# Optimization experiments

Measured on AMD Instinct MI355X. Metric: run time of the kernel, lower is better.

## Reference

```python
import jax, jax.numpy as jnp
import numpy as np

B, N, E, F, FE = 4, 10000, 160000, 128, 16  # batch, nodes, edges, filters(=node feat dim), edge feat dim
EPS = 1e-3  # keras LayerNormalization default epsilon


def layernorm(x, gamma, beta):
    mu = jnp.mean(x, axis=-1, keepdims=True)
    var = jnp.mean(jnp.square(x - mu), axis=-1, keepdims=True)
    return (x - mu) * jax.lax.rsqrt(var + EPS) * gamma + beta


def setup_inputs() -> dict:
    key = jax.random.key(0)
    ks = jax.random.split(key, 8)
    nodes = jax.random.normal(ks[0], (B, N, F), dtype=jnp.float32)
    edge_features = jax.random.normal(ks[1], (B, E, FE), dtype=jnp.float32)
    edges = jax.random.randint(ks[2], (B, E, 2), 0, N, dtype=jnp.int32)
    edge_weights = jax.random.uniform(ks[3], (B, E, 1), dtype=jnp.float32)
    edge_dropout = jnp.ones((B, E, 2), dtype=jnp.float32)
    W_msg = jax.random.normal(ks[4], (2 * F + FE, F), dtype=jnp.float32) * 0.02
    b_msg = jnp.zeros((F,), jnp.float32)
    g_msg = jnp.ones((F,), jnp.float32)
    beta_msg = jnp.zeros((F,), jnp.float32)
    W_upd = jax.random.normal(ks[5], (2 * F, F), dtype=jnp.float32) * 0.02
    b_upd = jnp.zeros((F,), jnp.float32)
    g_upd = jnp.ones((F,), jnp.float32)
    beta_upd = jnp.zeros((F,), jnp.float32)
    return dict(nodes=nodes, edge_features=edge_features, edges=edges,
                edge_weights=edge_weights, edge_dropout=edge_dropout,
                W_msg=W_msg, b_msg=b_msg, g_msg=g_msg, beta_msg=beta_msg,
                W_upd=W_upd, b_upd=b_upd, g_upd=g_upd, beta_upd=beta_upd)


def reference(nodes, edge_features, edges, edge_weights, edge_dropout,
              W_msg, b_msg, g_msg, beta_msg, W_upd, b_upd, g_upd, beta_upd):
    n = nodes.shape[1]
    # gather both endpoints per edge: [B,E,2,F] -> [B,E,2F]
    gathered = jax.vmap(lambda nd, ed: nd[ed])(nodes, edges)
    msg_in = gathered.reshape(gathered.shape[0], gathered.shape[1], -1)
    msg_in = jnp.concatenate([msg_in, edge_features], axis=-1)
    # message MLP: Dense + GELU + LayerNorm
    h = jnp.einsum('bei,io->beo', msg_in, W_msg) + b_msg
    messages = layernorm(jax.nn.gelu(h, approximate=False), g_msg, beta_msg)
    weighted_messages = messages * edge_weights
    # scatter-sum to destination nodes (edge[:,1]), masked by dropout col 1
    dropped = weighted_messages * edge_dropout[..., 1:2]
    dst = edges[..., 1]
    aggregated = jax.vmap(lambda m, d: jax.ops.segment_sum(m, d, num_segments=n))(dropped, dst)
    # update: concat + Dense + GELU + LayerNorm
    combined = jnp.concatenate([nodes, aggregated], axis=-1)
    u = jnp.einsum('bni,io->bno', combined, W_upd) + b_upd
    updated_nodes = layernorm(jax.nn.gelu(u, approximate=False), g_upd, beta_upd)
    return updated_nodes
```

## Files before the change

kernel.cpp:

```cpp
#include <hip/hip_runtime.h>
#include <hip/hip_bf16.h>
#include <hip/hip_fp16.h>

#define BATCH   4
#define NNODES  10000
#define NEDGES  160000
#define FDIM    128
#define FEDIM   16
#define LNEPS   1e-3f

typedef __attribute__((ext_vector_type(8))) short v8s;
typedef __attribute__((ext_vector_type(4))) float v4f;

#define AGG_BYTES   ((size_t)BATCH * NNODES * FDIM * 2)
#define P_OFF       AGG_BYTES
#define P_BYTES     ((size_t)BATCH * NNODES * 256 * 2)
#define WTCAT_OFF   (P_OFF + P_BYTES)
#define WTUPD_OFF   (WTCAT_OFF + (size_t)256 * 128 * 2)
#define W3T_OFF     (WTUPD_OFF + (size_t)128 * 256 * 2)

static __device__ __forceinline__ unsigned short f2bf(float f) {
    __hip_bfloat16 h = __float2bfloat16(f);
    return *reinterpret_cast<unsigned short*>(&h);
}
static __device__ __forceinline__ float bfbits2f(unsigned bits16) {
    return __uint_as_float(bits16 << 16);
}

static __device__ __forceinline__ float gelu_f(float x) {
    float z = 0.7978845608028654f * (x + 0.044715f * x * x * x);
    float e = __expf(2.0f * z);
    float t = 1.0f - 2.0f / (e + 1.0f);
    return 0.5f * x * (1.0f + t);
}

static __device__ __forceinline__ bool is_bf16_mode(const void* gflag) {
    return ((*reinterpret_cast<const unsigned*>(gflag)) & 0xFFFFu) != 0u;
}
static __device__ __forceinline__ float ld_f(const void* p, long i, bool bf) {
    return bf ? (float)reinterpret_cast<const __hip_bfloat16*>(p)[i]
              : reinterpret_cast<const float*>(p)[i];
}
static __device__ __forceinline__ uint4 pack8(const float* p) {
    float4 f0 = *reinterpret_cast<const float4*>(p);
    float4 f1 = *reinterpret_cast<const float4*>(p + 4);
    uint4 o;
    o.x = f2bf(f0.x) | ((unsigned)f2bf(f0.y) << 16);
    o.y = f2bf(f0.z) | ((unsigned)f2bf(f0.w) << 16);
    o.z = f2bf(f1.x) | ((unsigned)f2bf(f1.y) << 16);
    o.w = f2bf(f1.z) | ((unsigned)f2bf(f1.w) << 16);
    return o;
}
static __device__ __forceinline__ uint4 h8_to_bf8(uint4 u) {
    unsigned w[4] = {u.x, u.y, u.z, u.w};
    uint4 o; unsigned r[4];
    #pragma unroll
    for (int q = 0; q < 4; q++) {
        __half lo = *reinterpret_cast<const __half*>(&w[q]);
        unsigned short hib = (unsigned short)(w[q] >> 16);
        __half hi = *reinterpret_cast<const __half*>(&hib);
        r[q] = f2bf(__half2float(lo)) | ((unsigned)f2bf(__half2float(hi)) << 16);
    }
    o.x = r[0]; o.y = r[1]; o.z = r[2]; o.w = r[3];
    return o;
}

#define NCAT (256 * 128)
#define NUPD (128 * 256)
#define NW3  (128 * 32)
__global__ void prep_weights(const void* __restrict__ Wmsg, const void* __restrict__ Wupd,
                             const void* __restrict__ gflag,
                             unsigned short* __restrict__ WtCat,
                             unsigned short* __restrict__ WtUpd,
                             unsigned short* __restrict__ W3t) {
    bool bf = is_bf16_mode(gflag);
    int i = blockIdx.x * 256 + threadIdx.x;
    if (i < NCAT) {
        int n = i >> 7, k = i & 127;
        int src = (n < 128) ? (k * 128 + n) : ((128 + k) * 128 + (n - 128));
        WtCat[i] = bf ? reinterpret_cast<const unsigned short*>(Wmsg)[src]
                      : f2bf(reinterpret_cast<const float*>(Wmsg)[src]);
    } else if (i < NCAT + NUPD) {
        int j = i - NCAT;
        int n = j >> 8, c = j & 255;
        WtUpd[j] = bf ? reinterpret_cast<const unsigned short*>(Wupd)[c * 128 + n]
                      : f2bf(reinterpret_cast<const float*>(Wupd)[c * 128 + n]);
    } else if (i < NCAT + NUPD + NW3) {
        int j = i - NCAT - NUPD;
        int n = j >> 5, k = j & 31;
        W3t[j] = (k < 16) ? (bf ? reinterpret_cast<const unsigned short*>(Wmsg)[(256 + k) * 128 + n]
                                : f2bf(reinterpret_cast<const float*>(Wmsg)[(256 + k) * 128 + n]))
                          : (unsigned short)0;
    }
}

__global__ __launch_bounds__(256) void pg_kernel(
    const void* __restrict__ nodes,
    const void* __restrict__ bmsg,
    const void* __restrict__ gflag,
    const unsigned short* __restrict__ Wt,
    unsigned short*       __restrict__ P)
{
    const bool bf = is_bf16_mode(gflag);
    __shared__ unsigned short sW[128 * 40];
    __shared__ unsigned short sA[128 * 40];

    const int tid  = threadIdx.x;
    const int lane = tid & 63, wave = tid >> 6;
    const int c    = lane & 15, quad = lane >> 4;
    const int row0 = blockIdx.x * 128;
    const int half = blockIdx.y;
    const int NROWS = BATCH * NNODES;

    float bcol[8];
    #pragma unroll
    for (int nt = 0; nt < 8; nt++)
        bcol[nt] = (half == 0) ? ld_f(bmsg, nt * 16 + c, bf) : 0.f;

    v4f acc[2][8];
    #pragma unroll
    for (int mt = 0; mt < 2; mt++)
        #pragma unroll
        for (int nt = 0; nt < 8; nt++) { v4f z = {0.f, 0.f, 0.f, 0.f}; acc[mt][nt] = z; }

    for (int ks = 0; ks < 4; ks++) {
        #pragma unroll
        for (int q = tid; q < 512; q += 256) {
            int n = q >> 2, part = q & 3;
            *reinterpret_cast<uint4*>(&sW[n * 40 + part * 8]) =
                *reinterpret_cast<const uint4*>(Wt + (half * 128 + n) * 128 + ks * 32 + part * 8);
        }
        #pragma unroll
        for (int q = tid; q < 512; q += 256) {
            int t = q >> 2, part = q & 3;
            int row = row0 + t; if (row >= NROWS) row = NROWS - 1;
            long off = (size_t)row * FDIM + ks * 32 + part * 8;
            uint4 v = bf ? *reinterpret_cast<const uint4*>(reinterpret_cast<const unsigned short*>(nodes) + off)
                         : pack8(reinterpret_cast<const float*>(nodes) + off);
            *reinterpret_cast<uint4*>(&sA[t * 40 + part * 8]) = v;
        }
        __syncthreads();

        v8s a0 = *reinterpret_cast<const v8s*>(&sA[(wave * 32 + c) * 40 + quad * 8]);
        v8s a1 = *reinterpret_cast<const v8s*>(&sA[(wave * 32 + 16 + c) * 40 + quad * 8]);
        #pragma unroll
        for (int nt = 0; nt < 8; nt++) {
            v8s bfr = *reinterpret_cast<const v8s*>(&sW[(nt * 16 + c) * 40 + quad * 8]);
            acc[0][nt] = __builtin_amdgcn_mfma_f32_16x16x32_bf16(a0, bfr, acc[0][nt], 0, 0, 0);
            acc[1][nt] = __builtin_amdgcn_mfma_f32_16x16x32_bf16(a1, bfr, acc[1][nt], 0, 0, 0);
        }
        __syncthreads();
    }

    #pragma unroll
    for (int mt = 0; mt < 2; mt++)
        #pragma unroll
        for (int r = 0; r < 4; r++) {
            int row = row0 + wave * 32 + mt * 16 + quad * 4 + r;
            if (row < NROWS) {
                float v[8];
                #pragma unroll
                for (int nt = 0; nt < 8; nt++) v[nt] = acc[mt][nt][r] + bcol[nt];
                uint4 o;
                o.x = f2bf(v[0]) | ((unsigned)f2bf(v[1]) << 16);
                o.y = f2bf(v[2]) | ((unsigned)f2bf(v[3]) << 16);
                o.z = f2bf(v[4]) | ((unsigned)f2bf(v[5]) << 16);
                o.w = f2bf(v[6]) | ((unsigned)f2bf(v[7]) << 16);
                *reinterpret_cast<uint4*>(P + (size_t)row * 256 + half * 128 + c * 8) = o;
            }
        }
}

__global__ __launch_bounds__(256) void edge_kernel(
    const unsigned short* __restrict__ P,
    const void* __restrict__ efeat,
    const int*  __restrict__ edges,
    const void* __restrict__ ew,
    const void* __restrict__ ed,
    const unsigned short* __restrict__ W3t,
    const void* __restrict__ gmsg,
    const void* __restrict__ betamsg,
    __half*     __restrict__ agg)
{
    const bool bf = is_bf16_mode(gmsg);
    __shared__ int   sSrc[128], sDst[128];
    __shared__ float sWgt[128];

    const int tid  = threadIdx.x;
    const int b    = blockIdx.x / (NEDGES / 128);
    const int e0   = (blockIdx.x % (NEDGES / 128)) * 128;
    const int lane = tid & 63, wave = tid >> 6;
    const int c    = lane & 15, quad = lane >> 4;

    if (tid < 128) {
        long be = (long)b * NEDGES + e0 + tid;
        sSrc[tid] = edges[be * 2];
        sDst[tid] = edges[be * 2 + 1];
        sWgt[tid] = ld_f(ew, be, bf) * ld_f(ed, be * 2 + 1, bf);
    }

    float gcol[8], becol[8];
    #pragma unroll
    for (int nt = 0; nt < 8; nt++) {
        gcol[nt]  = ld_f(gmsg, nt * 16 + c, bf);
        becol[nt] = ld_f(betamsg, nt * 16 + c, bf);
    }

    v8s bfrag[8];
    #pragma unroll
    for (int nt = 0; nt < 8; nt++)
        bfrag[nt] = *reinterpret_cast<const v8s*>(W3t + (nt * 16 + c) * 32 + quad * 8);

    v4f acc[2][8];
    #pragma unroll
    for (int mt = 0; mt < 2; mt++)
        #pragma unroll
        for (int nt = 0; nt < 8; nt++) { v4f z = {0.f, 0.f, 0.f, 0.f}; acc[mt][nt] = z; }

    #pragma unroll
    for (int mt = 0; mt < 2; mt++) {
        v8s a = {0, 0, 0, 0, 0, 0, 0, 0};
        if (quad < 2) {
            long ebase = ((long)b * NEDGES + e0 + wave * 32 + mt * 16 + c) * FEDIM + quad * 8;
            if (bf) {
                uint4 u = *reinterpret_cast<const uint4*>(reinterpret_cast<const unsigned short*>(efeat) + ebase);
                a = *reinterpret_cast<v8s*>(&u);
            } else {
                uint4 u = pack8(reinterpret_cast<const float*>(efeat) + ebase);
                a = *reinterpret_cast<v8s*>(&u);
            }
        }
        #pragma unroll
        for (int nt = 0; nt < 8; nt++)
            acc[mt][nt] = __builtin_amdgcn_mfma_f32_16x16x32_bf16(a, bfrag[nt], acc[mt][nt], 0, 0, 0);
    }

    __syncthreads();

    const size_t nbase = (size_t)b * NNODES;
    const bool even = !(c & 1);

    #pragma unroll
    for (int mt = 0; mt < 2; mt++) {
        uint4 U1[4], U2[4];
        #pragma unroll
        for (int r = 0; r < 4; r++) {
            int m = wave * 32 + mt * 16 + quad * 4 + r;
            U1[r] = *reinterpret_cast<const uint4*>(P + (nbase + sSrc[m]) * 256 + c * 8);
            U2[r] = *reinterpret_cast<const uint4*>(P + (nbase + sDst[m]) * 256 + 128 + c * 8);
        }
        #pragma unroll
        for (int r = 0; r < 4; r++) {
            int m = wave * 32 + mt * 16 + quad * 4 + r;
            unsigned w1[4] = {U1[r].x, U1[r].y, U1[r].z, U1[r].w};
            unsigned w2[4] = {U2[r].x, U2[r].y, U2[r].z, U2[r].w};
            float h[8];
            #pragma unroll
            for (int q = 0; q < 4; q++) {
                h[q * 2]     = bfbits2f(w1[q] & 0xFFFFu) + bfbits2f(w2[q] & 0xFFFFu) + acc[mt][q * 2][r];
                h[q * 2 + 1] = __uint_as_float(w1[q] & 0xFFFF0000u) + __uint_as_float(w2[q] & 0xFFFF0000u)
                               + acc[mt][q * 2 + 1][r];
            }
            float s = 0.f, sq = 0.f;
            #pragma unroll
            for (int nt = 0; nt < 8; nt++) {
                float g = gelu_f(h[nt]);
                h[nt] = g; s += g; sq += g * g;
            }
            #pragma unroll
            for (int off = 1; off < 16; off <<= 1) {
                s  += __shfl_xor(s, off);
                sq += __shfl_xor(sq, off);
            }
            float mu  = s * (1.0f / 128.0f);
            float var = sq * (1.0f / 128.0f) - mu * mu;
            float rs  = rsqrtf(var + LNEPS);
            float wgt = sWgt[m];
            float y[8];
            #pragma unroll
            for (int nt = 0; nt < 8; nt++)
                y[nt] = ((h[nt] - mu) * rs * gcol[nt] + becol[nt]) * wgt;

            __half* aout = agg + (nbase + sDst[m]) * FDIM;
            #pragma unroll
            for (int np = 0; np < 4; np++) {
                int nt = np * 2;
                float t0 = __shfl_xor(y[nt], 1);
                float t1 = __shfl_xor(y[nt + 1], 1);
                __half2 v = even ? __floats2half2_rn(y[nt], t0)
                                 : __floats2half2_rn(t1, y[nt + 1]);
                int hoff = even ? (nt * 16 + c) : ((nt + 1) * 16 + c - 1);
                unsafeAtomicAdd(reinterpret_cast<__half2*>(aout + hoff), v);
            }
        }
    }
}

__global__ __launch_bounds__(256) void upd_kernel(
    const void* __restrict__ nodes,
    const __half* __restrict__ agg,
    const unsigned short* __restrict__ Wt,
    const void* __restrict__ bupd,
    const void* __restrict__ gupd,
    const void* __restrict__ beupd,
    void*       __restrict__ out)
{
    const bool bf = is_bf16_mode(gupd);
    __shared__ unsigned short sW[128 * 40];
    __shared__ unsigned short sA[64 * 40];

    const int tid  = threadIdx.x;
    const int lane = tid & 63, wave = tid >> 6;
    const int c    = lane & 15, quad = lane >> 4;
    const int row0 = blockIdx.x * 64;

    float bcol[8], gcol[8], becol[8];
    #pragma unroll
    for (int nt = 0; nt < 8; nt++) {
        int col = nt * 16 + c;
        bcol[nt]  = ld_f(bupd, col, bf);
        gcol[nt]  = ld_f(gupd, col, bf);
        becol[nt] = ld_f(beupd, col, bf);
    }

    v4f acc[8];
    #pragma unroll
    for (int nt = 0; nt < 8; nt++) { v4f z = {0.f, 0.f, 0.f, 0.f}; acc[nt] = z; }

    for (int ks = 0; ks < 8; ks++) {
        #pragma unroll
        for (int q = tid; q < 512; q += 256) {
            int n = q >> 2, part = q & 3;
            *reinterpret_cast<uint4*>(&sW[n * 40 + part * 8]) =
                *reinterpret_cast<const uint4*>(Wt + n * 256 + ks * 32 + part * 8);
        }
        {
            int t = tid >> 2, part = tid & 3;
            int row = row0 + t;
            uint4 v;
            if (ks < 4) {
                long off = (size_t)row * FDIM + ks * 32 + part * 8;
                v = bf ? *reinterpret_cast<const uint4*>(reinterpret_cast<const unsigned short*>(nodes) + off)
                       : pack8(reinterpret_cast<const float*>(nodes) + off);
            } else {
                uint4 u = *reinterpret_cast<const uint4*>(
                    reinterpret_cast<const unsigned short*>(agg) + (size_t)row * FDIM + (ks - 4) * 32 + part * 8);
                v = h8_to_bf8(u);
            }
            *reinterpret_cast<uint4*>(&sA[t * 40 + part * 8]) = v;
        }
        __syncthreads();

        v8s a0 = *reinterpret_cast<const v8s*>(&sA[(wave * 16 + c) * 40 + quad * 8]);
        #pragma unroll
        for (int nt = 0; nt < 8; nt++) {
            v8s bfr = *reinterpret_cast<const v8s*>(&sW[(nt * 16 + c) * 40 + quad * 8]);
            acc[nt] = __builtin_amdgcn_mfma_f32_16x16x32_bf16(a0, bfr, acc[nt], 0, 0, 0);
        }
        __syncthreads();
    }

    float s[4] = {0, 0, 0, 0}, sq[4] = {0, 0, 0, 0};
    #pragma unroll
    for (int nt = 0; nt < 8; nt++) {
        v4f v = acc[nt];
        #pragma unroll
        for (int r = 0; r < 4; r++) {
            float g = gelu_f(v[r] + bcol[nt]);
            v[r] = g;
            s[r] += g; sq[r] += g * g;
        }
        acc[nt] = v;
    }
    #pragma unroll
    for (int off = 1; off < 16; off <<= 1) {
        #pragma unroll
        for (int r = 0; r < 4; r++) {
            s[r]  += __shfl_xor(s[r], off);
            sq[r] += __shfl_xor(sq[r], off);
        }
    }
    #pragma unroll
    for (int r = 0; r < 4; r++) {
        float mu  = s[r] * (1.0f / 128.0f);
        float var = sq[r] * (1.0f / 128.0f) - mu * mu;
        float rs  = rsqrtf(var + LNEPS);
        int row = row0 + wave * 16 + quad * 4 + r;
        #pragma unroll
        for (int nt = 0; nt < 8; nt++) {
            float y = (acc[nt][r] - mu) * rs * gcol[nt] + becol[nt];
            size_t oi = (size_t)row * FDIM + nt * 16 + c;
            if (bf) reinterpret_cast<__hip_bfloat16*>(out)[oi] = __float2bfloat16(y);
            else    reinterpret_cast<float*>(out)[oi] = y;
        }
    }
}

extern "C" void kernel_launch(void* const* d_in, const int* in_sizes, int n_in,
                              void* d_out, int out_size, void* d_ws, size_t ws_size,
                              hipStream_t stream)
{
    const void* nodes   = d_in[0];
    const void* efeat   = d_in[1];
    const int*  edges   = (const int*)d_in[2];
    const void* ew      = d_in[3];
    const void* ed      = d_in[4];
    const void* Wmsg    = d_in[5];
    const void* bmsg    = d_in[6];
    const void* gmsg    = d_in[7];
    const void* betamsg = d_in[8];
    const void* Wupd    = d_in[9];
    const void* bupd    = d_in[10];
    const void* gupd    = d_in[11];
    const void* betaupd = d_in[12];

    char* ws = (char*)d_ws;
    __half* agg = (__half*)ws;
    unsigned short* P     = (unsigned short*)(ws + P_OFF);
    unsigned short* WtCat = (unsigned short*)(ws + WTCAT_OFF);
    unsigned short* WtUpd = (unsigned short*)(ws + WTUPD_OFF);
    unsigned short* W3t   = (unsigned short*)(ws + W3T_OFF);

    hipMemsetAsync(agg, 0, AGG_BYTES, stream);
    prep_weights<<<(NCAT + NUPD + NW3 + 255) / 256, 256, 0, stream>>>(
        Wmsg, Wupd, gmsg, WtCat, WtUpd, W3t);
    pg_kernel<<<dim3((BATCH * NNODES + 127) / 128, 2), 256, 0, stream>>>(
        nodes, bmsg, gmsg, WtCat, P);
    edge_kernel<<<BATCH * (NEDGES / 128), 256, 0, stream>>>(
        P, efeat, edges, ew, ed, W3t, gmsg, betamsg, agg);
    upd_kernel<<<BATCH * NNODES / 64, 256, 0, stream>>>(
        nodes, agg, WtUpd, bupd, gupd, betaupd, d_out);
}
```

Measured before the change: 289.4 us.

## Sort edges by destination and merge same-node messages before atomic scatter

Adds a per-call counting sort of edges by destination node (histogram, a single-block scan, and a scatter into packed per-edge records holding src, dst, weight and bf16 edge features). The edge kernel then reads the sorted records and keeps a per-thread running sum of consecutive messages that share a destination, flushing with half2 atomics only when the destination changes. The aim is fewer atomic collisions and better locality for the destination-row gathers and atomics. In exchange it adds three extra kernel launches, a serial single-block scan, another atomic pass over every edge, and writes and rereads of a 48-byte record per edge.

```diff
diff --git a/kernel.cpp b/kernel.cpp
--- a/kernel.cpp
+++ b/kernel.cpp
@@ -8,16 +8,23 @@
 #define FDIM    128
 #define FEDIM   16
 #define LNEPS   1e-3f
+#define NTOTE   (BATCH * NEDGES)
+#define NTOTN   (BATCH * NNODES)
 
 typedef __attribute__((ext_vector_type(8))) short v8s;
 typedef __attribute__((ext_vector_type(4))) float v4f;
 
-#define AGG_BYTES   ((size_t)BATCH * NNODES * FDIM * 2)
-#define P_OFF       AGG_BYTES
-#define P_BYTES     ((size_t)BATCH * NNODES * 256 * 2)
+#define AGG_BYTES   ((size_t)NTOTN * FDIM * 2)
+#define CNT_OFF     AGG_BYTES
+#define CNT_BYTES   ((size_t)NTOTN * 4)
+#define CUR_OFF     (CNT_OFF + CNT_BYTES)
+#define P_OFF       (CUR_OFF + CNT_BYTES)
+#define P_BYTES     ((size_t)NTOTN * 256 * 2)
 #define WTCAT_OFF   (P_OFF + P_BYTES)
 #define WTUPD_OFF   (WTCAT_OFF + (size_t)256 * 128 * 2)
 #define W3T_OFF     (WTUPD_OFF + (size_t)128 * 256 * 2)
+#define REC_OFF     (W3T_OFF + (size_t)128 * 32 * 2)
+#define ERECW       12
 
 static __device__ __forceinline__ unsigned short f2bf(float f) {
     __hip_bfloat16 h = __float2bfloat16(f);
@@ -94,6 +101,75 @@
     }
 }
 
+__global__ __launch_bounds__(256) void edge_hist(const int* __restrict__ edges,
+                                                 int* __restrict__ counts) {
+    int gid = blockIdx.x * 256 + threadIdx.x;
+    if (gid >= NTOTE) return;
+    int b = gid / NEDGES;
+    int dst = edges[(size_t)gid * 2 + 1];
+    atomicAdd(&counts[b * NNODES + dst], 1);
+}
+
+__global__ __launch_bounds__(1024) void scan_kernel(const int* __restrict__ counts,
+                                                    int* __restrict__ cursor) {
+    __shared__ int part[1024];
+    const int C = 40;
+    int tid = threadIdx.x;
+    int lo = tid * C;
+    int hi = lo + C; if (hi > NTOTN) hi = NTOTN;
+    int s = 0;
+    for (int i = lo; i < hi; i++) s += counts[i];
+    part[tid] = s;
+    __syncthreads();
+    for (int off = 1; off < 1024; off <<= 1) {
+        int v = (tid >= off) ? part[tid - off] : 0;
+        __syncthreads();
+        part[tid] += v;
+        __syncthreads();
+    }
+    int run = (tid > 0) ? part[tid - 1] : 0;
+    for (int i = lo; i < hi; i++) {
+        cursor[i] = run;
+        run += counts[i];
+    }
+}
+
+__global__ __launch_bounds__(256) void sort_scatter(
+    const int*  __restrict__ edges,
+    const void* __restrict__ ew,
+    const void* __restrict__ ed,
+    const void* __restrict__ efeat,
+    const void* __restrict__ gflag,
+    int*        __restrict__ cursor,
+    unsigned int* __restrict__ rec)
+{
+    const bool bf = is_bf16_mode(gflag);
+    int gid = blockIdx.x * 256 + threadIdx.x;
+    if (gid >= NTOTE) return;
+    int b = gid / NEDGES;
+    long be = gid;
+    int src = edges[be * 2];
+    int dst = edges[be * 2 + 1];
+    float w = ld_f(ew, be, bf) * ld_f(ed, be * 2 + 1, bf);
+    uint4 h0, h1;
+    if (bf) {
+        const unsigned short* ep = reinterpret_cast<const unsigned short*>(efeat) + be * FEDIM;
+        h0 = *reinterpret_cast<const uint4*>(ep);
+        h1 = *reinterpret_cast<const uint4*>(ep + 8);
+    } else {
+        const float* ep = reinterpret_cast<const float*>(efeat) + be * FEDIM;
+        h0 = pack8(ep);
+        h1 = pack8(ep + 8);
+    }
+    int pos = atomicAdd(&cursor[b * NNODES + dst], 1);
+    unsigned int* rp = rec + (size_t)pos * ERECW;
+    *reinterpret_cast<uint4*>(rp)     = make_uint4((unsigned)(b * NNODES + src),
+                                                   (unsigned)(b * NNODES + dst),
+                                                   __float_as_uint(w), 0u);
+    *reinterpret_cast<uint4*>(rp + 4) = h0;
+    *reinterpret_cast<uint4*>(rp + 8) = h1;
+}
+
 __global__ __launch_bounds__(256) void pg_kernel(
     const void* __restrict__ nodes,
     const void* __restrict__ bmsg,
@@ -173,10 +249,7 @@
 
 __global__ __launch_bounds__(256) void edge_kernel(
     const unsigned short* __restrict__ P,
-    const void* __restrict__ efeat,
-    const int*  __restrict__ edges,
-    const void* __restrict__ ew,
-    const void* __restrict__ ed,
+    const unsigned int*   __restrict__ rec,
     const unsigned short* __restrict__ W3t,
     const void* __restrict__ gmsg,
     const void* __restrict__ betamsg,
@@ -187,16 +260,15 @@
     __shared__ float sWgt[128];
 
     const int tid  = threadIdx.x;
-    const int b    = blockIdx.x / (NEDGES / 128);
-    const int e0   = (blockIdx.x % (NEDGES / 128)) * 128;
+    const int e0   = blockIdx.x * 128;
     const int lane = tid & 63, wave = tid >> 6;
     const int c    = lane & 15, quad = lane >> 4;
 
     if (tid < 128) {
-        long be = (long)b * NEDGES + e0 + tid;
-        sSrc[tid] = edges[be * 2];
-        sDst[tid] = edges[be * 2 + 1];
-        sWgt[tid] = ld_f(ew, be, bf) * ld_f(ed, be * 2 + 1, bf);
+        uint4 hh = *reinterpret_cast<const uint4*>(rec + (size_t)(e0 + tid) * ERECW);
+        sSrc[tid] = (int)hh.x;
+        sDst[tid] = (int)hh.y;
+        sWgt[tid] = __uint_as_float(hh.z);
     }
 
     float gcol[8], becol[8];
@@ -221,14 +293,9 @@
     for (int mt = 0; mt < 2; mt++) {
         v8s a = {0, 0, 0, 0, 0, 0, 0, 0};
         if (quad < 2) {
-            long ebase = ((long)b * NEDGES + e0 + wave * 32 + mt * 16 + c) * FEDIM + quad * 8;
-            if (bf) {
-                uint4 u = *reinterpret_cast<const uint4*>(reinterpret_cast<const unsigned short*>(efeat) + ebase);
-                a = *reinterpret_cast<v8s*>(&u);
-            } else {
-                uint4 u = pack8(reinterpret_cast<const float*>(efeat) + ebase);
-                a = *reinterpret_cast<v8s*>(&u);
-            }
+            int slot = e0 + wave * 32 + ((c >> 2) << 3) + mt * 4 + (c & 3);
+            uint4 u = *reinterpret_cast<const uint4*>(rec + (size_t)slot * ERECW + 4 + quad * 4);
+            a = *reinterpret_cast<v8s*>(&u);
         }
         #pragma unroll
         for (int nt = 0; nt < 8; nt++)
@@ -237,21 +304,36 @@
 
     __syncthreads();
 
-    const size_t nbase = (size_t)b * NNODES;
     const bool even = !(c & 1);
+    float racc[8];
+    int cur = -1;
+
+    auto flushv = [&](int dstrow) {
+        __half* aout = agg + (size_t)dstrow * FDIM;
+        #pragma unroll
+        for (int np = 0; np < 4; np++) {
+            int nt = np * 2;
+            float t0 = __shfl_xor(racc[nt], 1);
+            float t1 = __shfl_xor(racc[nt + 1], 1);
+            __half2 v = even ? __floats2half2_rn(racc[nt], t0)
+                             : __floats2half2_rn(t1, racc[nt + 1]);
+            int hoff = even ? (nt * 16 + c) : ((nt + 1) * 16 + c - 1);
+            unsafeAtomicAdd(reinterpret_cast<__half2*>(aout + hoff), v);
+        }
+    };
 
     #pragma unroll
     for (int mt = 0; mt < 2; mt++) {
         uint4 U1[4], U2[4];
         #pragma unroll
         for (int r = 0; r < 4; r++) {
-            int m = wave * 32 + mt * 16 + quad * 4 + r;
-            U1[r] = *reinterpret_cast<const uint4*>(P + (nbase + sSrc[m]) * 256 + c * 8);
-            U2[r] = *reinterpret_cast<const uint4*>(P + (nbase + sDst[m]) * 256 + 128 + c * 8);
+            int m = wave * 32 + quad * 8 + mt * 4 + r;
+            U1[r] = *reinterpret_cast<const uint4*>(P + (size_t)sSrc[m] * 256 + c * 8);
+            U2[r] = *reinterpret_cast<const uint4*>(P + (size_t)sDst[m] * 256 + 128 + c * 8);
         }
         #pragma unroll
         for (int r = 0; r < 4; r++) {
-            int m = wave * 32 + mt * 16 + quad * 4 + r;
+            int m = wave * 32 + quad * 8 + mt * 4 + r;
             unsigned w1[4] = {U1[r].x, U1[r].y, U1[r].z, U1[r].w};
             unsigned w2[4] = {U2[r].x, U2[r].y, U2[r].z, U2[r].w};
             float h[8];
@@ -276,24 +358,21 @@
             float var = sq * (1.0f / 128.0f) - mu * mu;
             float rs  = rsqrtf(var + LNEPS);
             float wgt = sWgt[m];
-            float y[8];
-            #pragma unroll
-            for (int nt = 0; nt < 8; nt++)
-                y[nt] = ((h[nt] - mu) * rs * gcol[nt] + becol[nt]) * wgt;
-
-            __half* aout = agg + (nbase + sDst[m]) * FDIM;
-            #pragma unroll
-            for (int np = 0; np < 4; np++) {
-                int nt = np * 2;
-                float t0 = __shfl_xor(y[nt], 1);
-                float t1 = __shfl_xor(y[nt + 1], 1);
-                __half2 v = even ? __floats2half2_rn(y[nt], t0)
-                                 : __floats2half2_rn(t1, y[nt + 1]);
-                int hoff = even ? (nt * 16 + c) : ((nt + 1) * 16 + c - 1);
-                unsafeAtomicAdd(reinterpret_cast<__half2*>(aout + hoff), v);
+            int d = sDst[m];
+            if (d != cur) {
+                if (cur >= 0) flushv(cur);
+                cur = d;
+                #pragma unroll
+                for (int nt = 0; nt < 8; nt++)
+                    racc[nt] = ((h[nt] - mu) * rs * gcol[nt] + becol[nt]) * wgt;
+            } else {
+                #pragma unroll
+                for (int nt = 0; nt < 8; nt++)
+                    racc[nt] += ((h[nt] - mu) * rs * gcol[nt] + becol[nt]) * wgt;
             }
         }
     }
+    flushv(cur);
 }
 
 __global__ __launch_bounds__(256) void upd_kernel(
@@ -415,19 +494,26 @@
     const void* betaupd = d_in[12];
 
     char* ws = (char*)d_ws;
-    __half* agg = (__half*)ws;
-    unsigned short* P     = (unsigned short*)(ws + P_OFF);
-    unsigned short* WtCat = (unsigned short*)(ws + WTCAT_OFF);
-    unsigned short* WtUpd = (unsigned short*)(ws + WTUPD_OFF);
-    unsigned short* W3t   = (unsigned short*)(ws + W3T_OFF);
-
-    hipMemsetAsync(agg, 0, AGG_BYTES, stream);
+    __half* agg          = (__half*)ws;
+    int*    counts       = (int*)(ws + CNT_OFF);
+    int*    cursor       = (int*)(ws + CUR_OFF);
+    unsigned short* P    = (unsigned short*)(ws + P_OFF);
+    unsigned short* WtCat= (unsigned short*)(ws + WTCAT_OFF);
+    unsigned short* WtUpd= (unsigned short*)(ws + WTUPD_OFF);
+    unsigned short* W3t  = (unsigned short*)(ws + W3T_OFF);
+    unsigned int*   rec  = (unsigned int*)(ws + REC_OFF);
+
+    hipMemsetAsync(agg, 0, AGG_BYTES + CNT_BYTES, stream);
     prep_weights<<<(NCAT + NUPD + NW3 + 255) / 256, 256, 0, stream>>>(
         Wmsg, Wupd, gmsg, WtCat, WtUpd, W3t);
-    pg_kernel<<<dim3((BATCH * NNODES + 127) / 128, 2), 256, 0, stream>>>(
+    pg_kernel<<<dim3((NTOTN + 127) / 128, 2), 256, 0, stream>>>(
         nodes, bmsg, gmsg, WtCat, P);
-    edge_kernel<<<BATCH * (NEDGES / 128), 256, 0, stream>>>(
-        P, efeat, edges, ew, ed, W3t, gmsg, betamsg, agg);
-    upd_kernel<<<BATCH * NNODES / 64, 256, 0, stream>>>(
+    edge_hist<<<(NTOTE + 255) / 256, 256, 0, stream>>>(edges, counts);
+    scan_kernel<<<1, 1024, 0, stream>>>(counts, cursor);
+    sort_scatter<<<(NTOTE + 255) / 256, 256, 0, stream>>>(
+        edges, ew, ed, efeat, gmsg, cursor, rec);
+    edge_kernel<<<NTOTE / 128, 256, 0, stream>>>(
+        P, rec, W3t, gmsg, betamsg, agg);
+    upd_kernel<<<NTOTN / 64, 256, 0, stream>>>(
         nodes, agg, WtUpd, bupd, gupd, betaupd, d_out);
 }
```

Result: slower. 385.7 us (+33.3%).
